# Performance work log

Measured on AMD Instinct MI355X. Metric: run time of the kernel, lower is better.

The kernel has to match this reference:

```python
import jax, jax.numpy as jnp
import numpy as np

ALPHA = 0.2
TAU = 1.0  # max(tau_init, 1e-6)
K_CAP = 256 - 1  # cluster_size_max - 1
SCORE_DIM = 256
PROJ = 64
TH_HIDDEN = 128
THETA_IN = 512


def setup_inputs() -> dict:
    key = jax.random.key(0)
    ks = jax.random.split(key, 12)
    B, N, D = 4, 4096, SCORE_DIM
    x = jax.random.normal(ks[0], (B, N, D), dtype=jnp.float32)
    # sparse-ish binary adjacency, stored dense (as the torch module densifies it)
    adj = (jax.random.uniform(ks[1], (B, N, N)) < 0.005).astype(jnp.float32)
    seed_ctx_feats = jax.random.normal(ks[2], (B, 384), dtype=jnp.float32)
    local_stats = jax.random.normal(ks[3], (B, 128), dtype=jnp.float32)
    cluster_mask = (jax.random.uniform(ks[4], (B, N)) < 0.01).astype(jnp.float32)
    cand_mask = (jax.random.uniform(ks[5], (B, N)) < 0.5).astype(jnp.float32)
    s = 1.0 / np.sqrt(D)
    Wq = jax.random.normal(ks[6], (D, PROJ), dtype=jnp.float32) * s
    Wk = jax.random.normal(ks[7], (D, PROJ), dtype=jnp.float32) * s
    th_w1 = jax.random.normal(ks[8], (THETA_IN, TH_HIDDEN), dtype=jnp.float32) * (1.0 / np.sqrt(THETA_IN))
    th_b1 = jnp.zeros((TH_HIDDEN,), dtype=jnp.float32)
    th_w2 = jax.random.normal(ks[9], (TH_HIDDEN, 1), dtype=jnp.float32) * (1.0 / np.sqrt(TH_HIDDEN))
    th_b2 = jnp.zeros((1,), dtype=jnp.float32)
    return {"x": x, "adj": adj, "seed_ctx_feats": seed_ctx_feats,
            "local_stats": local_stats, "cluster_mask": cluster_mask,
            "cand_mask": cand_mask, "Wq": Wq, "Wk": Wk,
            "th_w1": th_w1, "th_b1": th_b1, "th_w2": th_w2, "th_b2": th_b2}


def reference(x, adj, seed_ctx_feats, local_stats, cluster_mask, cand_mask,
              Wq, Wk, th_w1, th_b1, th_w2, th_b2):
    B, N, D = x.shape
    x_k = x @ Wk  # [B, N, 64]
    # seed_repr is None -> take seed node from argmax of cluster_mask
    seed_idx = jnp.argmax(cluster_mask, axis=-1)            # [B]
    q = x[jnp.arange(B), seed_idx] @ Wq                      # [B, 64]
    scores = jnp.einsum('bnp,bp->bn', x_k, q) / jnp.sqrt(jnp.float32(PROJ))
    # edges-to-cluster count and degree (dense adjacency matvec / row-sum)
    e2c = jnp.einsum('bnm,bm->bn', adj, cluster_mask)        # [B, N]
    deg = jnp.maximum(adj.sum(axis=-1), 1.0)                 # [B, N]
    cand_scores = scores + ALPHA * (e2c / deg)
    # threshold head MLP
    theta_in = jnp.concatenate([seed_ctx_feats, local_stats], axis=-1)  # [B, 512]
    h = jax.nn.relu(theta_in @ th_w1 + th_b1)
    theta = (h @ th_w2 + th_b2)[:, 0]                        # [B]
    logits = (cand_scores - theta[:, None]) / TAU
    p = jax.nn.sigmoid(logits) * cand_mask                   # [B, N]
    # soft cap: if more than K_CAP nodes exceed 0.5, keep only top-K_CAP probs
    over = jax.lax.stop_gradient((p > 0.5).astype(p.dtype).sum(axis=-1) - K_CAP)
    need_trim = over > 0                                     # [B]
    _, topk_idx = jax.lax.top_k(p, K_CAP)                    # [B, K_CAP]
    keep = jnp.zeros_like(p).at[jnp.arange(B)[:, None], topk_idx].set(1.0)
    p = jnp.where(need_trim[:, None], p * keep, p)
    # straight-through hard gate
    hard = (p > 0.5).astype(p.dtype) + p - jax.lax.stop_gradient(p)
    expected_size = jax.lax.stop_gradient(p.sum(axis=-1))
    mean_p = jax.lax.stop_gradient(p.mean(axis=-1))
    return hard, p, theta, expected_size, mean_p
```

## Files before the change

kernel.cpp:

```cpp
#include <hip/hip_runtime.h>
#include <math.h>

#define B 4
#define N 4096
#define D 256
#define PROJ 64
#define TH_HIDDEN 128
#define K_CAP 255
#define ALPHA 0.2f
#define ROWS_PER_BLOCK 8
#define BLOCKS_PER_BATCH (N / ROWS_PER_BLOCK)

typedef float floatx4 __attribute__((ext_vector_type(4)));


__global__ __launch_bounds__(256) void prep_kernel(
    const float* __restrict__ x, const float* __restrict__ cluster_mask,
    const float* __restrict__ seed_ctx, const float* __restrict__ local_stats,
    const float* __restrict__ Wq, const float* __restrict__ Wk,
    const float* __restrict__ th_w1, const float* __restrict__ th_b1,
    const float* __restrict__ th_w2, const float* __restrict__ th_b2,
    float* v_ws, float* theta_out)
{
    const int bb = blockIdx.x;
    const int t = threadIdx.x;

    if (bb >= B) {
        const int b = bb - B;
        __shared__ float s_in[512];
        __shared__ float s_part[256];

        for (int i = t; i < 384; i += 256) s_in[i] = seed_ctx[b * 384 + i];
        if (t < 128) s_in[384 + t] = local_stats[b * 128 + t];
        __syncthreads();

        {
            const int j = t & 127;
            const int h = t >> 7;
            const float* w1 = th_w1 + (size_t)(h * 256) * TH_HIDDEN + j;
            const float* xin = s_in + h * 256;
            float acc = 0.f;
            #pragma unroll 8
            for (int i = 0; i < 256; ++i)
                acc += xin[i] * w1[i * TH_HIDDEN];
            s_part[t] = acc;
        }
        __syncthreads();
        if (t < TH_HIDDEN)
            s_part[t] = fmaxf(s_part[t] + s_part[t + 128] + th_b1[t], 0.f);
        __syncthreads();
        if (t < 64) {
            float a2 = s_part[t] * th_w2[t] + s_part[t + 64] * th_w2[t + 64];
            for (int off = 32; off > 0; off >>= 1)
                a2 += __shfl_down(a2, off, 64);
            if (t == 0) theta_out[b] = a2 + th_b2[0];
        }
        return;
    }

    const int b = bb;
    __shared__ float s_red[256];
    __shared__ int   s_idx[256];
    __shared__ float s_xseed[D];
    __shared__ float s_part[256];
    __shared__ float s_r[PROJ];

    float bestv = -1e30f; int besti = 0;
    for (int i = t; i < N; i += 256) {
        float vv = cluster_mask[b * N + i];
        if (vv > bestv) { bestv = vv; besti = i; }
    }
    s_red[t] = bestv; s_idx[t] = besti;
    __syncthreads();
    for (int s = 128; s > 0; s >>= 1) {
        if (t < s) {
            float v2 = s_red[t + s]; int i2 = s_idx[t + s];
            if (v2 > s_red[t] || (v2 == s_red[t] && i2 < s_idx[t])) {
                s_red[t] = v2; s_idx[t] = i2;
            }
        }
        __syncthreads();
    }
    const int seed = s_idx[0];

    s_xseed[t] = x[(size_t)b * N * D + (size_t)seed * D + t];
    __syncthreads();

    {
        const int j = t & 63;
        const int q = t >> 6;
        const float* wq = Wq + (size_t)(q * 64) * PROJ + j;
        const float* xs = s_xseed + q * 64;
        float acc = 0.f;
        #pragma unroll 8
        for (int d = 0; d < 64; ++d)
            acc += xs[d] * wq[d * PROJ];
        s_part[t] = acc;
    }
    __syncthreads();
    if (t < PROJ)
        s_r[t] = s_part[t] + s_part[t + 64] + s_part[t + 128] + s_part[t + 192];
    __syncthreads();

    {
        const float4* wk = (const float4*)(Wk + (size_t)t * PROJ);
        float acc = 0.f;
        #pragma unroll
        for (int j4 = 0; j4 < PROJ / 4; ++j4) {
            float4 w = wk[j4];
            float4 r4 = *(const float4*)&s_r[j4 * 4];
            acc += w.x * r4.x + w.y * r4.y + w.z * r4.z + w.w * r4.w;
        }
        v_ws[b * D + t] = acc * 0.125f;
    }
}

__global__ __launch_bounds__(256) void score_kernel(
    const float* __restrict__ x, const float* __restrict__ adj,
    const float* __restrict__ cluster_mask, const float* __restrict__ cand_mask,
    const float* __restrict__ v_ws, const float* __restrict__ theta_ws,
    float* __restrict__ p_ws)
{
    const int b = blockIdx.x / BLOCKS_PER_BATCH;
    const int chunk = blockIdx.x % BLOCKS_PER_BATCH;
    const int t = threadIdx.x;
    const int wave = t >> 6;
    const int lane = t & 63;

    __shared__ float s_mask[N];
    __shared__ float s_v[D];

    for (int i = t * 4; i < N; i += 1024)
        *(float4*)&s_mask[i] = *(const float4*)&cluster_mask[b * N + i];
    if (t < D) s_v[t] = v_ws[b * D + t];
    __syncthreads();

    const float theta = theta_ws[b];
    const int row0 = chunk * ROWS_PER_BLOCK;

    const int n0 = row0 + wave;
    const int n1 = n0 + 4;
    const float* arow0 = adj + (size_t)b * N * N + (size_t)n0 * N;
    const float* arow1 = adj + (size_t)b * N * N + (size_t)n1 * N;

    float deg0 = 0.f, e2c0 = 0.f, deg1 = 0.f, e2c1 = 0.f;
    #pragma unroll
    for (int k = 0; k < N / 256; ++k) {
        const int i = lane * 4 + k * 256;
        floatx4 a0 = __builtin_nontemporal_load((const floatx4*)&arow0[i]);
        floatx4 a1 = __builtin_nontemporal_load((const floatx4*)&arow1[i]);
        float4 m = *(const float4*)&s_mask[i];
        deg0 += a0.x + a0.y + a0.z + a0.w;
        e2c0 += a0.x * m.x + a0.y * m.y + a0.z * m.z + a0.w * m.w;
        deg1 += a1.x + a1.y + a1.z + a1.w;
        e2c1 += a1.x * m.x + a1.y * m.y + a1.z * m.z + a1.w * m.w;
    }
    float sc0, sc1;
    {
        const float* xrow0 = x + (size_t)b * N * D + (size_t)n0 * D;
        const float* xrow1 = x + (size_t)b * N * D + (size_t)n1 * D;
        float4 xv0 = *(const float4*)&xrow0[lane * 4];
        float4 xv1 = *(const float4*)&xrow1[lane * 4];
        float4 vv  = *(const float4*)&s_v[lane * 4];
        sc0 = xv0.x * vv.x + xv0.y * vv.y + xv0.z * vv.z + xv0.w * vv.w;
        sc1 = xv1.x * vv.x + xv1.y * vv.y + xv1.z * vv.z + xv1.w * vv.w;
    }
    for (int off = 32; off > 0; off >>= 1) {
        deg0 += __shfl_down(deg0, off, 64);
        e2c0 += __shfl_down(e2c0, off, 64);
        sc0  += __shfl_down(sc0,  off, 64);
        deg1 += __shfl_down(deg1, off, 64);
        e2c1 += __shfl_down(e2c1, off, 64);
        sc1  += __shfl_down(sc1,  off, 64);
    }
    if (lane == 0) {
        float d0 = fmaxf(deg0, 1.0f);
        float cand0 = sc0 + ALPHA * (e2c0 / d0);
        float p0 = cand_mask[b * N + n0] / (1.f + expf(-(cand0 - theta)));
        p_ws[b * N + n0] = p0;
        float d1 = fmaxf(deg1, 1.0f);
        float cand1 = sc1 + ALPHA * (e2c1 / d1);
        float p1 = cand_mask[b * N + n1] / (1.f + expf(-(cand1 - theta)));
        p_ws[b * N + n1] = p1;
    }
}

__global__ __launch_bounds__(256) void finalize_kernel(float* p_in, float* out)
{
    const int b = blockIdx.x;
    const int t = threadIdx.x;
    __shared__ float        sp[N];
    __shared__ unsigned int hist[256];
    __shared__ float        s_red[256];
    __shared__ unsigned int s_cnt[256];
    __shared__ unsigned int s_scan[256];
    __shared__ unsigned int s_bcast[2];

    for (int i = t * 4; i < N; i += 1024)
        *(float4*)&sp[i] = *(const float4*)&p_in[b * N + i];
    __syncthreads();

    {
        unsigned int c = 0;
        for (int i = t; i < N; i += 256) c += (sp[i] > 0.5f) ? 1u : 0u;
        s_cnt[t] = c;
    }
    __syncthreads();
    for (int s = 128; s > 0; s >>= 1) { if (t < s) s_cnt[t] += s_cnt[t + s]; __syncthreads(); }
    const unsigned int over_cnt = s_cnt[0];
    __syncthreads();
    const bool need_trim = over_cnt > K_CAP;

    unsigned int prefix = 0u;
    unsigned int k_rem = K_CAP;
    if (need_trim) {
        for (int pass = 0; pass < 4; ++pass) {
            const int shift = 24 - pass * 8;
            const unsigned int himask = (pass == 0) ? 0u : (0xFFFFFFFFu << (shift + 8));
            hist[t] = 0u;
            __syncthreads();
            for (int i = t; i < N; i += 256) {
                unsigned int u = __float_as_uint(sp[i]);
                if ((u & himask) == prefix)
                    atomicAdd(&hist[(u >> shift) & 255u], 1u);
            }
            __syncthreads();
            s_scan[t] = hist[t];
            __syncthreads();
            for (int off = 1; off < 256; off <<= 1) {
                unsigned int add = (t + off < 256) ? s_scan[t + off] : 0u;
                __syncthreads();
                s_scan[t] += add;
                __syncthreads();
            }
            const unsigned int Ginc = s_scan[t];
            const unsigned int G = Ginc - hist[t];
            if (G < k_rem && k_rem <= Ginc) {
                s_bcast[0] = prefix | ((unsigned int)t << shift);
                s_bcast[1] = k_rem - G;
            }
            __syncthreads();
            prefix = s_bcast[0];
            k_rem  = s_bcast[1];
            __syncthreads();
        }
    }
    const float vk = __uint_as_float(prefix);
    const unsigned int t_keep = k_rem;

    unsigned int tie_excl = 0;
    if (need_trim) {
        unsigned int local_tie = 0;
        const int base = t * 16;
        for (int j = 0; j < 16; ++j)
            local_tie += (__float_as_uint(sp[base + j]) == prefix) ? 1u : 0u;
        s_cnt[t] = local_tie;
        __syncthreads();
        s_scan[t] = local_tie;
        __syncthreads();
        for (int off = 1; off < 256; off <<= 1) {
            unsigned int add = (t >= off) ? s_scan[t - off] : 0u;
            __syncthreads();
            s_scan[t] += add;
            __syncthreads();
        }
        tie_excl = s_scan[t] - s_cnt[t];
        __syncthreads();
    }

    float psum = 0.f;
    {
        const int base = t * 16;
        unsigned int tie_rank = tie_excl;
        for (int j = 0; j < 16; ++j) {
            const int i = base + j;
            float p = sp[i];
            if (need_trim) {
                const unsigned int u = __float_as_uint(p);
                bool keep;
                if (u == prefix) { keep = (tie_rank < t_keep); tie_rank++; }
                else             { keep = (p > vk); }
                if (!keep) p = 0.f;
            }
            out[b * N + i]         = (p > 0.5f) ? 1.0f : 0.0f;
            out[B * N + b * N + i] = p;
            psum += p;
        }
    }
    s_red[t] = psum;
    __syncthreads();
    for (int s = 128; s > 0; s >>= 1) { if (t < s) s_red[t] += s_red[t + s]; __syncthreads(); }
    if (t == 0) {
        out[2 * B * N + B + b]     = s_red[0];
        out[2 * B * N + 2 * B + b] = s_red[0] * (1.0f / N);
    }
}

extern "C" void kernel_launch(void* const* d_in, const int* in_sizes, int n_in,
                              void* d_out, int out_size, void* d_ws, size_t ws_size,
                              hipStream_t stream) {
    const float* x            = (const float*)d_in[0];
    const float* adj          = (const float*)d_in[1];
    const float* seed_ctx     = (const float*)d_in[2];
    const float* local_stats  = (const float*)d_in[3];
    const float* cluster_mask = (const float*)d_in[4];
    const float* cand_mask    = (const float*)d_in[5];
    const float* Wq           = (const float*)d_in[6];
    const float* Wk           = (const float*)d_in[7];
    const float* th_w1        = (const float*)d_in[8];
    const float* th_b1        = (const float*)d_in[9];
    const float* th_w2        = (const float*)d_in[10];
    const float* th_b2        = (const float*)d_in[11];
    float* out = (float*)d_out;

    float* v_ws     = out;
    float* p_ws     = out + B * N;
    float* theta_ws = out + 2 * B * N;

    hipLaunchKernelGGL(prep_kernel, dim3(2 * B), dim3(256), 0, stream,
                       x, cluster_mask, seed_ctx, local_stats, Wq, Wk,
                       th_w1, th_b1, th_w2, th_b2, v_ws, theta_ws);
    hipLaunchKernelGGL(score_kernel, dim3(B * BLOCKS_PER_BATCH), dim3(256), 0, stream,
                       x, adj, cluster_mask, cand_mask, v_ws, theta_ws, p_ws);
    hipLaunchKernelGGL(finalize_kernel, dim3(B), dim3(256), 0, stream,
                       p_ws, out);
}
```

Measured before the change: 400.5 us.

## Fuse prep into score kernel and use wave-shuffle reductions in finalize

Removes the separate prep kernel: every score block now recomputes the seed argmax, the query projection, the Wk fold and the threshold MLP itself, then proceeds to the adjacency pass. This saves one launch and the serial dependency on a tiny 8-block kernel. The price is redundant per-block work, about 2048 blocks each reading Wq, Wk and th_w1 (roughly 0.3MB per block from L2), which could add noticeable time before the streaming adj loads start. The finalize kernel's shared-memory tree reductions and scans are replaced with wave shuffles, cutting barriers.

```diff
diff --git a/kernel.cpp b/kernel.cpp
--- a/kernel.cpp
+++ b/kernel.cpp
@@ -14,92 +14,99 @@
 typedef float floatx4 __attribute__((ext_vector_type(4)));
 
 
-__global__ __launch_bounds__(256) void prep_kernel(
-    const float* __restrict__ x, const float* __restrict__ cluster_mask,
+__global__ __launch_bounds__(256) void score_kernel(
+    const float* __restrict__ x, const float* __restrict__ adj,
+    const float* __restrict__ cluster_mask, const float* __restrict__ cand_mask,
     const float* __restrict__ seed_ctx, const float* __restrict__ local_stats,
     const float* __restrict__ Wq, const float* __restrict__ Wk,
     const float* __restrict__ th_w1, const float* __restrict__ th_b1,
     const float* __restrict__ th_w2, const float* __restrict__ th_b2,
-    float* v_ws, float* theta_out)
+    float* __restrict__ p_ws, float* __restrict__ theta_out)
 {
-    const int bb = blockIdx.x;
+    const int b = blockIdx.x / BLOCKS_PER_BATCH;
+    const int chunk = blockIdx.x % BLOCKS_PER_BATCH;
     const int t = threadIdx.x;
-
-    if (bb >= B) {
-        const int b = bb - B;
-        __shared__ float s_in[512];
-        __shared__ float s_part[256];
-
-        for (int i = t; i < 384; i += 256) s_in[i] = seed_ctx[b * 384 + i];
-        if (t < 128) s_in[384 + t] = local_stats[b * 128 + t];
-        __syncthreads();
-
-        {
-            const int j = t & 127;
-            const int h = t >> 7;
-            const float* w1 = th_w1 + (size_t)(h * 256) * TH_HIDDEN + j;
-            const float* xin = s_in + h * 256;
-            float acc = 0.f;
+    const int wave = t >> 6;
+    const int lane = t & 63;
+
+    __shared__ float s_mask[N];
+    __shared__ float s_v[D];
+    __shared__ float s_xh[256];
+    __shared__ float s_mlp[256];
+    __shared__ float s_r[PROJ];
+    __shared__ float s_argv[4];
+    __shared__ int   s_argi[4];
+    __shared__ float s_theta;
+
+    for (int i = t * 4; i < N; i += 1024)
+        *(float4*)&s_mask[i] = *(const float4*)&cluster_mask[b * N + i];
+    __syncthreads();
+
+    {
+        float bestv = -1e30f; int besti = 0;
+        for (int i = t; i < N; i += 256) {
+            float vv = s_mask[i];
+            if (vv > bestv) { bestv = vv; besti = i; }
+        }
+        for (int off = 32; off; off >>= 1) {
+            float v2 = __shfl_down(bestv, off, 64);
+            int   i2 = __shfl_down(besti, off, 64);
+            if (v2 > bestv || (v2 == bestv && i2 < besti)) { bestv = v2; besti = i2; }
+        }
+        if (lane == 0) { s_argv[wave] = bestv; s_argi[wave] = besti; }
+    }
+    __syncthreads();
+    if (t == 0) {
+        float bv = s_argv[0]; int bi = s_argi[0];
+        #pragma unroll
+        for (int w = 1; w < 4; ++w) {
+            float v2 = s_argv[w]; int i2 = s_argi[w];
+            if (v2 > bv || (v2 == bv && i2 < bi)) { bv = v2; bi = i2; }
+        }
+        s_argi[0] = bi;
+    }
+    __syncthreads();
+    const int seed = s_argi[0];
+
+    s_xh[t] = x[(size_t)b * N * D + (size_t)seed * D + t];
+    {
+        const int j = t & 127;
+        const int h = t >> 7;
+        const float* w1 = th_w1 + (size_t)(h * 256) * TH_HIDDEN + j;
+        float acc = 0.f;
+        if (h == 0) {
+            const float* sc = seed_ctx + b * 384;
             #pragma unroll 8
-            for (int i = 0; i < 256; ++i)
-                acc += xin[i] * w1[i * TH_HIDDEN];
-            s_part[t] = acc;
-        }
-        __syncthreads();
-        if (t < TH_HIDDEN)
-            s_part[t] = fmaxf(s_part[t] + s_part[t + 128] + th_b1[t], 0.f);
-        __syncthreads();
-        if (t < 64) {
-            float a2 = s_part[t] * th_w2[t] + s_part[t + 64] * th_w2[t + 64];
-            for (int off = 32; off > 0; off >>= 1)
-                a2 += __shfl_down(a2, off, 64);
-            if (t == 0) theta_out[b] = a2 + th_b2[0];
-        }
-        return;
-    }
-
-    const int b = bb;
-    __shared__ float s_red[256];
-    __shared__ int   s_idx[256];
-    __shared__ float s_xseed[D];
-    __shared__ float s_part[256];
-    __shared__ float s_r[PROJ];
-
-    float bestv = -1e30f; int besti = 0;
-    for (int i = t; i < N; i += 256) {
-        float vv = cluster_mask[b * N + i];
-        if (vv > bestv) { bestv = vv; besti = i; }
-    }
-    s_red[t] = bestv; s_idx[t] = besti;
-    __syncthreads();
-    for (int s = 128; s > 0; s >>= 1) {
-        if (t < s) {
-            float v2 = s_red[t + s]; int i2 = s_idx[t + s];
-            if (v2 > s_red[t] || (v2 == s_red[t] && i2 < s_idx[t])) {
-                s_red[t] = v2; s_idx[t] = i2;
-            }
-        }
-        __syncthreads();
-    }
-    const int seed = s_idx[0];
-
-    s_xseed[t] = x[(size_t)b * N * D + (size_t)seed * D + t];
-    __syncthreads();
-
-    {
-        const int j = t & 63;
-        const int q = t >> 6;
+            for (int i = 0; i < 256; ++i) acc += sc[i] * w1[i * TH_HIDDEN];
+        } else {
+            const float* sc = seed_ctx + b * 384 + 256;
+            #pragma unroll 8
+            for (int i = 0; i < 128; ++i) acc += sc[i] * w1[i * TH_HIDDEN];
+            const float* ls = local_stats + b * 128;
+            const float* w1b = w1 + 128 * TH_HIDDEN;
+            #pragma unroll 8
+            for (int i = 0; i < 128; ++i) acc += ls[i] * w1b[i * TH_HIDDEN];
+        }
+        s_mlp[t] = acc;
+    }
+    __syncthreads();
+
+    {
+        const int j = (wave << 4) + (lane >> 2);
+        const int q = lane & 3;
+        const float* xs = s_xh + q * 64;
         const float* wq = Wq + (size_t)(q * 64) * PROJ + j;
-        const float* xs = s_xseed + q * 64;
         float acc = 0.f;
         #pragma unroll 8
-        for (int d = 0; d < 64; ++d)
-            acc += xs[d] * wq[d * PROJ];
-        s_part[t] = acc;
-    }
-    __syncthreads();
-    if (t < PROJ)
-        s_r[t] = s_part[t] + s_part[t + 64] + s_part[t + 128] + s_part[t + 192];
+        for (int d = 0; d < 64; ++d) acc += xs[d] * wq[d * PROJ];
+        acc += __shfl_xor(acc, 1, 64);
+        acc += __shfl_xor(acc, 2, 64);
+        if (q == 0) s_r[j] = acc;
+    }
+    __syncthreads();
+
+    if (t < TH_HIDDEN)
+        s_xh[t] = fmaxf(s_mlp[t] + s_mlp[t + 128] + th_b1[t], 0.f);
     __syncthreads();
 
     {
@@ -111,31 +118,18 @@
             float4 r4 = *(const float4*)&s_r[j4 * 4];
             acc += w.x * r4.x + w.y * r4.y + w.z * r4.z + w.w * r4.w;
         }
-        v_ws[b * D + t] = acc * 0.125f;
-    }
-}
-
-__global__ __launch_bounds__(256) void score_kernel(
-    const float* __restrict__ x, const float* __restrict__ adj,
-    const float* __restrict__ cluster_mask, const float* __restrict__ cand_mask,
-    const float* __restrict__ v_ws, const float* __restrict__ theta_ws,
-    float* __restrict__ p_ws)
-{
-    const int b = blockIdx.x / BLOCKS_PER_BATCH;
-    const int chunk = blockIdx.x % BLOCKS_PER_BATCH;
-    const int t = threadIdx.x;
-    const int wave = t >> 6;
-    const int lane = t & 63;
-
-    __shared__ float s_mask[N];
-    __shared__ float s_v[D];
-
-    for (int i = t * 4; i < N; i += 1024)
-        *(float4*)&s_mask[i] = *(const float4*)&cluster_mask[b * N + i];
-    if (t < D) s_v[t] = v_ws[b * D + t];
-    __syncthreads();
-
-    const float theta = theta_ws[b];
+        s_v[t] = acc * 0.125f;
+    }
+    if (wave == 1) {
+        float a2 = s_xh[lane] * th_w2[lane] + s_xh[lane + 64] * th_w2[lane + 64];
+        for (int off = 32; off; off >>= 1) a2 += __shfl_down(a2, off, 64);
+        if (lane == 0) s_theta = a2 + th_b2[0];
+    }
+    __syncthreads();
+
+    if (chunk == 0 && t == 0) theta_out[b] = s_theta;
+
+    const float theta = s_theta;
     const int row0 = chunk * ROWS_PER_BLOCK;
 
     const int n0 = row0 + wave;
@@ -189,11 +183,12 @@
 {
     const int b = blockIdx.x;
     const int t = threadIdx.x;
+    const int wave = t >> 6;
+    const int lane = t & 63;
     __shared__ float        sp[N];
     __shared__ unsigned int hist[256];
-    __shared__ float        s_red[256];
-    __shared__ unsigned int s_cnt[256];
-    __shared__ unsigned int s_scan[256];
+    __shared__ unsigned int s_ured[4];
+    __shared__ float        s_wred[4];
     __shared__ unsigned int s_bcast[2];
 
     for (int i = t * 4; i < N; i += 1024)
@@ -203,13 +198,13 @@
     {
         unsigned int c = 0;
         for (int i = t; i < N; i += 256) c += (sp[i] > 0.5f) ? 1u : 0u;
-        s_cnt[t] = c;
-    }
-    __syncthreads();
-    for (int s = 128; s > 0; s >>= 1) { if (t < s) s_cnt[t] += s_cnt[t + s]; __syncthreads(); }
-    const unsigned int over_cnt = s_cnt[0];
-    __syncthreads();
+        for (int off = 32; off; off >>= 1) c += __shfl_down(c, off, 64);
+        if (lane == 0) s_ured[wave] = c;
+    }
+    __syncthreads();
+    const unsigned int over_cnt = s_ured[0] + s_ured[1] + s_ured[2] + s_ured[3];
     const bool need_trim = over_cnt > K_CAP;
+    __syncthreads();
 
     unsigned int prefix = 0u;
     unsigned int k_rem = K_CAP;
@@ -225,19 +220,36 @@
                     atomicAdd(&hist[(u >> shift) & 255u], 1u);
             }
             __syncthreads();
-            s_scan[t] = hist[t];
-            __syncthreads();
-            for (int off = 1; off < 256; off <<= 1) {
-                unsigned int add = (t + off < 256) ? s_scan[t + off] : 0u;
-                __syncthreads();
-                s_scan[t] += add;
-                __syncthreads();
-            }
-            const unsigned int Ginc = s_scan[t];
-            const unsigned int G = Ginc - hist[t];
-            if (G < k_rem && k_rem <= Ginc) {
-                s_bcast[0] = prefix | ((unsigned int)t << shift);
-                s_bcast[1] = k_rem - G;
+            if (wave == 0) {
+                const unsigned int h0 = hist[lane * 4 + 0];
+                const unsigned int h1 = hist[lane * 4 + 1];
+                const unsigned int h2 = hist[lane * 4 + 2];
+                const unsigned int h3 = hist[lane * 4 + 3];
+                const unsigned int s3 = h3, s2 = h2 + s3, s1 = h1 + s2, s0 = h0 + s1;
+                unsigned int incl = s0;
+                for (int off = 1; off < 64; off <<= 1) {
+                    unsigned int o = __shfl_down(incl, off, 64);
+                    if (lane + off < 64) incl += o;
+                }
+                const unsigned int tail = incl - s0;
+                const unsigned int gi0 = tail + s0, gi1 = tail + s1,
+                                   gi2 = tail + s2, gi3 = tail + s3;
+                if (gi0 - h0 < k_rem && k_rem <= gi0) {
+                    s_bcast[0] = prefix | ((unsigned int)(lane * 4 + 0) << shift);
+                    s_bcast[1] = k_rem - (gi0 - h0);
+                }
+                if (gi1 - h1 < k_rem && k_rem <= gi1) {
+                    s_bcast[0] = prefix | ((unsigned int)(lane * 4 + 1) << shift);
+                    s_bcast[1] = k_rem - (gi1 - h1);
+                }
+                if (gi2 - h2 < k_rem && k_rem <= gi2) {
+                    s_bcast[0] = prefix | ((unsigned int)(lane * 4 + 2) << shift);
+                    s_bcast[1] = k_rem - (gi2 - h2);
+                }
+                if (gi3 - h3 < k_rem && k_rem <= gi3) {
+                    s_bcast[0] = prefix | ((unsigned int)(lane * 4 + 3) << shift);
+                    s_bcast[1] = k_rem - (gi3 - h3);
+                }
             }
             __syncthreads();
             prefix = s_bcast[0];
@@ -254,18 +266,16 @@
         const int base = t * 16;
         for (int j = 0; j < 16; ++j)
             local_tie += (__float_as_uint(sp[base + j]) == prefix) ? 1u : 0u;
-        s_cnt[t] = local_tie;
+        unsigned int incl = local_tie;
+        for (int off = 1; off < 64; off <<= 1) {
+            unsigned int o = __shfl_up(incl, off, 64);
+            if (lane >= off) incl += o;
+        }
+        if (lane == 63) s_ured[wave] = incl;
         __syncthreads();
-        s_scan[t] = local_tie;
-        __syncthreads();
-        for (int off = 1; off < 256; off <<= 1) {
-            unsigned int add = (t >= off) ? s_scan[t - off] : 0u;
-            __syncthreads();
-            s_scan[t] += add;
-            __syncthreads();
-        }
-        tie_excl = s_scan[t] - s_cnt[t];
-        __syncthreads();
+        unsigned int woff = 0;
+        for (int w = 0; w < wave; ++w) woff += s_ured[w];
+        tie_excl = woff + incl - local_tie;
     }
 
     float psum = 0.f;
@@ -287,12 +297,13 @@
             psum += p;
         }
     }
-    s_red[t] = psum;
-    __syncthreads();
-    for (int s = 128; s > 0; s >>= 1) { if (t < s) s_red[t] += s_red[t + s]; __syncthreads(); }
+    for (int off = 32; off; off >>= 1) psum += __shfl_down(psum, off, 64);
+    if (lane == 0) s_wred[wave] = psum;
+    __syncthreads();
     if (t == 0) {
-        out[2 * B * N + B + b]     = s_red[0];
-        out[2 * B * N + 2 * B + b] = s_red[0] * (1.0f / N);
+        const float tot = s_wred[0] + s_wred[1] + s_wred[2] + s_wred[3];
+        out[2 * B * N + B + b]     = tot;
+        out[2 * B * N + 2 * B + b] = tot * (1.0f / N);
     }
 }
 
@@ -313,15 +324,12 @@
     const float* th_b2        = (const float*)d_in[11];
     float* out = (float*)d_out;
 
-    float* v_ws     = out;
     float* p_ws     = out + B * N;
     float* theta_ws = out + 2 * B * N;
 
-    hipLaunchKernelGGL(prep_kernel, dim3(2 * B), dim3(256), 0, stream,
-                       x, cluster_mask, seed_ctx, local_stats, Wq, Wk,
-                       th_w1, th_b1, th_w2, th_b2, v_ws, theta_ws);
     hipLaunchKernelGGL(score_kernel, dim3(B * BLOCKS_PER_BATCH), dim3(256), 0, stream,
-                       x, adj, cluster_mask, cand_mask, v_ws, theta_ws, p_ws);
+                       x, adj, cluster_mask, cand_mask, seed_ctx, local_stats,
+                       Wq, Wk, th_w1, th_b1, th_w2, th_b2, p_ws, theta_ws);
     hipLaunchKernelGGL(finalize_kernel, dim3(B), dim3(256), 0, stream,
                        p_ws, out);
 }
```

Measured after the change: 421.4 us. 5.2% more time.
